# Performance work log

Measured on AMD Instinct MI355X. Metric: run time of the kernel, lower is better.

The kernel has to match this reference:

```python
import jax, jax.numpy as jnp
import numpy as np

NBLOCKS = 4
BATCH = 16384
DIMS = [(3072, 3000), (3000, 1000), (1000, 100), (100, 10)]


def _monarch_linear(x, w1, w2, bias, out_features):
    # x: (b, n); w1: (k, q, p) block-diag factor 1; w2: (l, s, r) block-diag factor 2
    b = x.shape[0]
    k, q, p = w1.shape
    l, s, r = w2.shape
    n_ext = k * p
    if x.shape[1] < n_ext:  # pad input up to in_features_extended
        x = jnp.pad(x, ((0, 0), (0, n_ext - x.shape[1])))
    xr = x.reshape(b, k, p)
    out1 = jnp.einsum('kqp,bkp->bkq', w1, xr)          # block-diag matmul 1
    # monarch permutation: flatten (k,q) -> view as (r,l) -> transpose to (l,r)
    out1 = out1.reshape(b, r, l).transpose(0, 2, 1)    # (b, l, r)
    out2 = jnp.einsum('lsr,blr->bls', w2, out1)        # block-diag matmul 2
    out = out2.reshape(b, l * s)[:, :out_features]     # truncate to out_features
    return out + bias


def _layer_shapes(fin, fout, nb):
    in_blk = -(-fin // nb)
    out_blk = -(-fout // nb)
    if in_blk * nb < out_blk * nb:
        return (nb, in_blk, in_blk), (nb, out_blk, in_blk)
    return (nb, out_blk, in_blk), (nb, out_blk, out_blk)


def setup_inputs() -> dict:
    key = jax.random.key(0)
    ks = jax.random.split(key, 16)
    inp = {"x": jax.random.normal(ks[0], (BATCH, DIMS[0][0]), jnp.float32)}
    i = 1
    for li, (fin, fout) in enumerate(DIMS, 1):
        s1, s2 = _layer_shapes(fin, fout, NBLOCKS)
        inp[f"w1_{li}"] = jax.random.normal(ks[i], s1, jnp.float32) / np.float32(np.sqrt(s1[2])); i += 1
        inp[f"w2_{li}"] = jax.random.normal(ks[i], s2, jnp.float32) / np.float32(np.sqrt(s2[2])); i += 1
        inp[f"b{li}"] = jnp.zeros((fout,), jnp.float32)
    return inp


def reference(x, w1_1, w2_1, b1, w1_2, w2_2, b2, w1_3, w2_3, b3, w1_4, w2_4, b4):
    h = x.reshape(x.shape[0], -1)
    h = jax.nn.relu(_monarch_linear(h, w1_1, w2_1, b1, 3000))
    h = jax.nn.relu(_monarch_linear(h, w1_2, w2_2, b2, 1000))
    h = jax.nn.relu(_monarch_linear(h, w1_3, w2_3, b3, 100))
    h = _monarch_linear(h, w1_4, w2_4, b4, 10)
    return jax.nn.log_softmax(h, axis=1)
```

## Files before the change

kernel.cpp:

```cpp
#include <hip/hip_runtime.h>
#include <stdint.h>
#include <math.h>

typedef unsigned short ushort_t;
typedef short short8 __attribute__((ext_vector_type(8)));
typedef float f32x4 __attribute__((ext_vector_type(4)));

__device__ __forceinline__ float b2f(ushort_t u) {
  union { uint32_t i; float f; } v; v.i = ((uint32_t)u) << 16; return v.f;
}
__device__ __forceinline__ ushort_t f2b(float f) {
  union { float f; uint32_t i; } v; v.f = f;
  uint32_t r = (v.i + 0x7FFFu + ((v.i >> 16) & 1u)) >> 16;
  return (ushort_t)r;
}

__device__ __forceinline__ void gload16(const void* g, void* l) {
  __builtin_amdgcn_global_load_lds(
      (const __attribute__((address_space(1))) void*)(uintptr_t)g,
      (__attribute__((address_space(3))) void*)(uint32_t)(uintptr_t)l,
      16, 0, 0);
}

__global__ void cast_f32_bf16(const float* __restrict__ src, ushort_t* __restrict__ dst, long n) {
  long stride = (long)gridDim.x * blockDim.x;
  for (long i = (long)blockIdx.x * blockDim.x + threadIdx.x; i * 8 < n; i += stride) {
    const float4* s = (const float4*)(src + i * 8);
    float4 a = s[0], b = s[1];
    short8 o;
    o[0] = (short)f2b(a.x); o[1] = (short)f2b(a.y); o[2] = (short)f2b(a.z); o[3] = (short)f2b(a.w);
    o[4] = (short)f2b(b.x); o[5] = (short)f2b(b.y); o[6] = (short)f2b(b.z); o[7] = (short)f2b(b.w);
    *(short8*)(dst + i * 8) = o;
  }
}

__global__ void cast_pad_w(const float* __restrict__ src, ushort_t* __restrict__ dst,
                           int NB, int Q, int P, int Qpad, int Ppad) {
  long total = (long)NB * Qpad * Ppad;
  for (long i = (long)blockIdx.x * blockDim.x + threadIdx.x; i < total;
       i += (long)gridDim.x * blockDim.x) {
    int p = (int)(i % Ppad);
    long t = i / Ppad;
    int q = (int)(t % Qpad);
    int b = (int)(t / Qpad);
    float v = (q < Q && p < P) ? src[((long)b * Q + q) * P + p] : 0.f;
    dst[i] = f2b(v);
  }
}

#define BM 128
#define BN 128
#define BK 64

template <int MODE>
__global__ __launch_bounds__(256, 2)
void gemm_bt(const ushort_t* __restrict__ A, int lda, long aZ,
             const ushort_t* __restrict__ W, int Npad, int Ppad, int K,
             const float* __restrict__ bias,
             ushort_t* __restrict__ out,
             int Q, int Rpad, long planeElems, int Spad, int ldout) {
  __shared__ __align__(16) ushort_t As[BM * BK];
  __shared__ __align__(16) ushort_t Bs[BN * BK];
  const int tid = threadIdx.x;
  const int lane = tid & 63;
  const int wave = tid >> 6;
  const int wm = wave >> 1, wn = wave & 1;
  const int z = blockIdx.z;
  const long m0 = (long)blockIdx.x * BM;
  const int n0 = blockIdx.y * BN;

  const ushort_t* Ab = A + (long)z * aZ + m0 * lda;
  const ushort_t* Wb = W + (long)z * Npad * Ppad + (long)n0 * Ppad;

  f32x4 acc[4][4] = {};

  for (int kt = 0; kt < K; kt += BK) {
#pragma unroll
    for (int i = 0; i < 4; ++i) {
      int ch = tid + i * 256;
      int r = ch >> 3;
      int c = (ch & 7) * 8;
      gload16(Ab + (long)r * lda + kt + c, &As[ch * 8]);
      gload16(Wb + (long)r * Ppad + kt + c, &Bs[ch * 8]);
    }
    __syncthreads();
#pragma unroll
    for (int kk = 0; kk < 2; ++kk) {
      short8 af[4], bf[4];
#pragma unroll
      for (int mi = 0; mi < 4; ++mi) {
        int row = wm * 64 + mi * 16 + (lane & 15);
        af[mi] = *(const short8*)&As[row * 64 + kk * 32 + ((lane >> 4) << 3)];
      }
#pragma unroll
      for (int nj = 0; nj < 4; ++nj) {
        int row = wn * 64 + nj * 16 + (lane & 15);
        bf[nj] = *(const short8*)&Bs[row * 64 + kk * 32 + ((lane >> 4) << 3)];
      }
#pragma unroll
      for (int mi = 0; mi < 4; ++mi)
#pragma unroll
        for (int nj = 0; nj < 4; ++nj)
          acc[mi][nj] = __builtin_amdgcn_mfma_f32_16x16x32_bf16(af[mi], bf[nj], acc[mi][nj], 0, 0, 0);
    }
    __syncthreads();
  }

  const int fq = lane >> 4;
  const int fr = lane & 15;
  if constexpr (MODE == 0) {
#pragma unroll
    for (int nj = 0; nj < 4; ++nj) {
      int q = n0 + wn * 64 + nj * 16 + fr;
      if (q < Q) {
        int f = z * Q + q;
        ushort_t* op = out + (long)(f & 3) * planeElems + (f >> 2);
#pragma unroll
        for (int mi = 0; mi < 4; ++mi) {
          long row = m0 + wm * 64 + mi * 16 + fq * 4;
#pragma unroll
          for (int j = 0; j < 4; ++j)
            op[(row + j) * (long)Rpad] = f2b(acc[mi][nj][j]);
        }
      }
    }
  } else {
#pragma unroll
    for (int nj = 0; nj < 4; ++nj) {
      int s = n0 + wn * 64 + nj * 16 + fr;
      if (s < Q) {
        float bv = bias[z * Q + s];
        ushort_t* op = out + (long)z * Spad + s;
#pragma unroll
        for (int mi = 0; mi < 4; ++mi) {
          long row = m0 + wm * 64 + mi * 16 + fq * 4;
#pragma unroll
          for (int j = 0; j < 4; ++j) {
            float v = acc[mi][nj][j] + bv;
            v = v > 0.f ? v : 0.f;
            op[(row + j) * (long)ldout] = f2b(v);
          }
        }
      }
    }
  }
}

__global__ __launch_bounds__(256)
void l4_softmax(const ushort_t* __restrict__ h3,
                const float* __restrict__ w14, const float* __restrict__ w24,
                const float* __restrict__ b4, float* __restrict__ outp) {
  __shared__ float w14s[300], w24s[36], b4s[10];
  int tid = threadIdx.x;
  for (int i = tid; i < 300; i += 256) w14s[i] = w14[i];
  if (tid < 36) w24s[tid] = w24[tid];
  if (tid < 10) b4s[tid] = b4[tid];
  __syncthreads();

  long row = (long)blockIdx.x * 256 + tid;
  const ushort_t* hr = h3 + row * 128;

  float a4[12];
#pragma unroll
  for (int k = 0; k < 4; ++k) {
    float hx[25];
#pragma unroll
    for (int p = 0; p < 25; ++p) hx[p] = b2f(hr[k * 32 + p]);
#pragma unroll
    for (int q = 0; q < 3; ++q) {
      float s = 0.f;
#pragma unroll
      for (int p = 0; p < 25; ++p) s += hx[p] * w14s[(k * 3 + q) * 25 + p];
      a4[k * 3 + q] = s;
    }
  }
  float logit[10];
#pragma unroll
  for (int l = 0; l < 4; ++l) {
#pragma unroll
    for (int s = 0; s < 3; ++s) {
      int j = l * 3 + s;
      if (j < 10) {
        float v = 0.f;
#pragma unroll
        for (int r = 0; r < 3; ++r) v += w24s[(l * 3 + s) * 3 + r] * a4[4 * r + l];
        logit[j] = v + b4s[j];
      }
    }
  }
  float m = logit[0];
#pragma unroll
  for (int j = 1; j < 10; ++j) m = fmaxf(m, logit[j]);
  float sum = 0.f;
#pragma unroll
  for (int j = 0; j < 10; ++j) sum += expf(logit[j] - m);
  float lse = m + logf(sum);
#pragma unroll
  for (int j = 0; j < 10; ++j) outp[row * 10 + j] = logit[j] - lse;
}

extern "C" void kernel_launch(void* const* d_in, const int* in_sizes, int n_in,
                              void* d_out, int out_size, void* d_ws, size_t ws_size,
                              hipStream_t stream) {
  (void)in_sizes; (void)n_in; (void)out_size; (void)ws_size;
  const float* x   = (const float*)d_in[0];
  const float* w11 = (const float*)d_in[1];
  const float* w21 = (const float*)d_in[2];
  const float* b1  = (const float*)d_in[3];
  const float* w12 = (const float*)d_in[4];
  const float* w22 = (const float*)d_in[5];
  const float* b2  = (const float*)d_in[6];
  const float* w13 = (const float*)d_in[7];
  const float* w23 = (const float*)d_in[8];
  const float* b3  = (const float*)d_in[9];
  const float* w14 = (const float*)d_in[10];
  const float* w24 = (const float*)d_in[11];
  const float* b4  = (const float*)d_in[12];
  float* out = (float*)d_out;
  char* ws = (char*)d_ws;

  ushort_t* w1b1 = (ushort_t*)(ws + 0);
  ushort_t* w2b1 = (ushort_t*)(ws + 4718592);
  ushort_t* w1b2 = (ushort_t*)(ws + 9437184);
  ushort_t* w2b2 = (ushort_t*)(ws + 11010048);
  ushort_t* w13b = (ushort_t*)(ws + 11534336);
  ushort_t* w23b = (ushort_t*)(ws + 11796480);
  const long OFF_XB = 11862016;
  ushort_t* xb = (ushort_t*)(ws + OFF_XB);
  ushort_t* t2 = (ushort_t*)(ws + OFF_XB);
  ushort_t* h2 = (ushort_t*)(ws + OFF_XB + 33554432);
  ushort_t* t3 = (ushort_t*)(ws + OFF_XB + 67108864);
  ushort_t* h3 = (ushort_t*)(ws + OFF_XB + 75497472);
  ushort_t* t1 = (ushort_t*)(ws + 112525312);
  ushort_t* h1 = (ushort_t*)(ws + 213188608);

  cast_f32_bf16<<<4096, 256, 0, stream>>>(x, xb, 50331648L);
  cast_pad_w<<<2048, 256, 0, stream>>>(w11, w1b1, 4, 750, 768, 768, 768);
  cast_pad_w<<<2048, 256, 0, stream>>>(w21, w2b1, 4, 750, 750, 768, 768);
  cast_pad_w<<<1024, 256, 0, stream>>>(w12, w1b2, 4, 250, 750, 256, 768);
  cast_pad_w<<<512, 256, 0, stream>>>(w22, w2b2, 4, 250, 250, 256, 256);
  cast_pad_w<<<256, 256, 0, stream>>>(w13, w13b, 4, 25, 250, 128, 256);
  cast_pad_w<<<128, 256, 0, stream>>>(w23, w23b, 4, 25, 25, 128, 64);

  gemm_bt<0><<<dim3(128, 6, 4), 256, 0, stream>>>(xb, 3072, 768L, w1b1, 768, 768, 768,
                                                  nullptr, t1, 750, 768, 16384L * 768, 0, 0);
  gemm_bt<1><<<dim3(128, 6, 4), 256, 0, stream>>>(t1, 768, 16384L * 768, w2b1, 768, 768, 768,
                                                  b1, h1, 750, 0, 0, 768, 3072);
  gemm_bt<0><<<dim3(128, 2, 4), 256, 0, stream>>>(h1, 3072, 768L, w1b2, 256, 768, 768,
                                                  nullptr, t2, 250, 256, 16384L * 256, 0, 0);
  gemm_bt<1><<<dim3(128, 2, 4), 256, 0, stream>>>(t2, 256, 16384L * 256, w2b2, 256, 256, 256,
                                                  b2, h2, 250, 0, 0, 256, 1024);
  gemm_bt<0><<<dim3(128, 1, 4), 256, 0, stream>>>(h2, 1024, 256L, w13b, 128, 256, 256,
                                                  nullptr, t3, 25, 64, 16384L * 64, 0, 0);
  gemm_bt<1><<<dim3(128, 1, 4), 256, 0, stream>>>(t3, 64, 16384L * 64, w23b, 128, 64, 64,
                                                  b3, h3, 25, 0, 0, 32, 128);
  l4_softmax<<<64, 256, 0, stream>>>(h3, w14, w24, b4, out);
}
```

Measured before the change: 719.0 us.

## Double-buffer LDS tiles in GEMM and swizzle block order across XCDs

The GEMM kernel now keeps two LDS buffers and issues the async global-to-LDS loads for the next K tile before computing on the current one, so memory transfer can overlap with MFMA work. It also launches a flat 1D grid and remaps block IDs with a stride-8 swizzle, presumably so neighbouring tiles that share A rows land on the same XCD's L2. LDS use doubles to 64KB per block, which may reduce occupancy below the launch-bounds target of 2 blocks per CU. The synchronisation placement in the unseen tail of the loop determines whether the overlap is race-free.

```diff
diff --git a/kernel.cpp b/kernel.cpp
--- a/kernel.cpp
+++ b/kernel.cpp
@@ -58,44 +58,63 @@
              const ushort_t* __restrict__ W, int Npad, int Ppad, int K,
              const float* __restrict__ bias,
              ushort_t* __restrict__ out,
-             int Q, int Rpad, long planeElems, int Spad, int ldout) {
-  __shared__ __align__(16) ushort_t As[BM * BK];
-  __shared__ __align__(16) ushort_t Bs[BN * BK];
+             int Q, int Rpad, long planeElems, int Spad, int ldout,
+             int gx, int gy) {
+  __shared__ __align__(16) ushort_t As[2][BM * BK];
+  __shared__ __align__(16) ushort_t Bs[2][BN * BK];
   const int tid = threadIdx.x;
   const int lane = tid & 63;
   const int wave = tid >> 6;
   const int wm = wave >> 1, wn = wave & 1;
-  const int z = blockIdx.z;
-  const long m0 = (long)blockIdx.x * BM;
-  const int n0 = blockIdx.y * BN;
+
+  const int nb = gridDim.x;
+  const int bid = blockIdx.x;
+  const int swz = (bid & 7) * (nb >> 3) + (bid >> 3);
+  const int bx = swz % gx;
+  const int rest = swz / gx;
+  const int by = rest % gy;
+  const int z = rest / gy;
+
+  const long m0 = (long)bx * BM;
+  const int n0 = by * BN;
 
   const ushort_t* Ab = A + (long)z * aZ + m0 * lda;
   const ushort_t* Wb = W + (long)z * Npad * Ppad + (long)n0 * Ppad;
 
   f32x4 acc[4][4] = {};
 
-  for (int kt = 0; kt < K; kt += BK) {
+  const int nsteps = K / BK;
+
+  auto stage = [&](int b, int kt) {
 #pragma unroll
     for (int i = 0; i < 4; ++i) {
       int ch = tid + i * 256;
       int r = ch >> 3;
       int c = (ch & 7) * 8;
-      gload16(Ab + (long)r * lda + kt + c, &As[ch * 8]);
-      gload16(Wb + (long)r * Ppad + kt + c, &Bs[ch * 8]);
-    }
-    __syncthreads();
+      gload16(Ab + (long)r * lda + kt + c, &As[b][ch * 8]);
+      gload16(Wb + (long)r * Ppad + kt + c, &Bs[b][ch * 8]);
+    }
+  };
+
+  stage(0, 0);
+  __syncthreads();
+
+  for (int it = 0; it < nsteps; ++it) {
+    const int cur = it & 1;
+    if (it + 1 < nsteps) stage(cur ^ 1, (it + 1) * BK);
+
 #pragma unroll
     for (int kk = 0; kk < 2; ++kk) {
       short8 af[4], bf[4];
 #pragma unroll
       for (int mi = 0; mi < 4; ++mi) {
         int row = wm * 64 + mi * 16 + (lane & 15);
-        af[mi] = *(const short8*)&As[row * 64 + kk * 32 + ((lane >> 4) << 3)];
+        af[mi] = *(const short8*)&As[cur][row * 64 + kk * 32 + ((lane >> 4) << 3)];
       }
 #pragma unroll
       for (int nj = 0; nj < 4; ++nj) {
         int row = wn * 64 + nj * 16 + (lane & 15);
-        bf[nj] = *(const short8*)&Bs[row * 64 + kk * 32 + ((lane >> 4) << 3)];
+        bf[nj] = *(const short8*)&Bs[cur][row * 64 + kk * 32 + ((lane >> 4) << 3)];
       }
 #pragma unroll
       for (int mi = 0; mi < 4; ++mi)
@@ -242,17 +261,17 @@
   cast_pad_w<<<256, 256, 0, stream>>>(w13, w13b, 4, 25, 250, 128, 256);
   cast_pad_w<<<128, 256, 0, stream>>>(w23, w23b, 4, 25, 25, 128, 64);
 
-  gemm_bt<0><<<dim3(128, 6, 4), 256, 0, stream>>>(xb, 3072, 768L, w1b1, 768, 768, 768,
-                                                  nullptr, t1, 750, 768, 16384L * 768, 0, 0);
-  gemm_bt<1><<<dim3(128, 6, 4), 256, 0, stream>>>(t1, 768, 16384L * 768, w2b1, 768, 768, 768,
-                                                  b1, h1, 750, 0, 0, 768, 3072);
-  gemm_bt<0><<<dim3(128, 2, 4), 256, 0, stream>>>(h1, 3072, 768L, w1b2, 256, 768, 768,
-                                                  nullptr, t2, 250, 256, 16384L * 256, 0, 0);
-  gemm_bt<1><<<dim3(128, 2, 4), 256, 0, stream>>>(t2, 256, 16384L * 256, w2b2, 256, 256, 256,
-                                                  b2, h2, 250, 0, 0, 256, 1024);
-  gemm_bt<0><<<dim3(128, 1, 4), 256, 0, stream>>>(h2, 1024, 256L, w13b, 128, 256, 256,
-                                                  nullptr, t3, 25, 64, 16384L * 64, 0, 0);
-  gemm_bt<1><<<dim3(128, 1, 4), 256, 0, stream>>>(t3, 64, 16384L * 64, w23b, 128, 64, 64,
-                                                  b3, h3, 25, 0, 0, 32, 128);
+  gemm_bt<0><<<128 * 6 * 4, 256, 0, stream>>>(xb, 3072, 768L, w1b1, 768, 768, 768,
+                                              nullptr, t1, 750, 768, 16384L * 768, 0, 0, 128, 6);
+  gemm_bt<1><<<128 * 6 * 4, 256, 0, stream>>>(t1, 768, 16384L * 768, w2b1, 768, 768, 768,
+                                              b1, h1, 750, 0, 0, 768, 3072, 128, 6);
+  gemm_bt<0><<<128 * 2 * 4, 256, 0, stream>>>(h1, 3072, 768L, w1b2, 256, 768, 768,
+                                              nullptr, t2, 250, 256, 16384L * 256, 0, 0, 128, 2);
+  gemm_bt<1><<<128 * 2 * 4, 256, 0, stream>>>(t2, 256, 16384L * 256, w2b2, 256, 256, 256,
+                                              b2, h2, 250, 0, 0, 256, 1024, 128, 2);
+  gemm_bt<0><<<128 * 1 * 4, 256, 0, stream>>>(h2, 1024, 256L, w13b, 128, 256, 256,
+                                              nullptr, t3, 25, 64, 16384L * 64, 0, 0, 128, 1);
+  gemm_bt<1><<<128 * 1 * 4, 256, 0, stream>>>(t3, 64, 16384L * 64, w23b, 128, 64, 64,
+                                              b3, h3, 25, 0, 0, 32, 128, 128, 1);
   l4_softmax<<<64, 256, 0, stream>>>(h3, w14, w24, b4, out);
 }
```

Measured after the change: 768.7 us. 6.9% more time.

## Add 256x256-tile GEMM with 4-slot LDS ring and swizzled layout for layers 1-2

Applied to the files above, without the earlier changes.

Adds a new GEMM kernel using 512 threads and 256x256 output tiles, fed by a 4-deep ring buffer of 32-wide K slices loaded directly into LDS, with an XOR-swizzled chunk layout to avoid bank conflicts. The four large block-diagonal matmuls of layers 1 and 2 switch to it. The intent is to raise arithmetic intensity per tile and hide global load latency through deeper prefetch. In exchange it uses 128KB of LDS per block and a large accumulator register footprint, which limits occupancy, and it gives fewer blocks for the smaller layer-2 GEMMs.

```diff
diff --git a/kernel.cpp b/kernel.cpp
--- a/kernel.cpp
+++ b/kernel.cpp
@@ -20,6 +20,17 @@
       (const __attribute__((address_space(1))) void*)(uintptr_t)g,
       (__attribute__((address_space(3))) void*)(uint32_t)(uintptr_t)l,
       16, 0, 0);
+}
+
+__device__ __forceinline__ int swz_chunk(int r, int c) {
+  int rp = (r >> 1) & 7;
+  int s8 = ((r & 1) << 2) | c;
+  return ((r >> 4) << 6) | (rp << 3) | (s8 ^ rp);
+}
+__device__ __forceinline__ void inv_chunk(int p, int& r, int& c) {
+  int rp = (p >> 3) & 7, ps = p & 7, s8 = ps ^ rp;
+  r = ((p >> 6) << 4) | (rp << 1) | (s8 >> 2);
+  c = s8 & 3;
 }
 
 __global__ void cast_f32_bf16(const float* __restrict__ src, ushort_t* __restrict__ dst, long n) {
@@ -45,6 +56,121 @@
     int b = (int)(t / Qpad);
     float v = (q < Q && p < P) ? src[((long)b * Q + q) * P + p] : 0.f;
     dst[i] = f2b(v);
+  }
+}
+
+template <int MODE>
+__global__ __launch_bounds__(512, 2)
+void gemm_ring(const ushort_t* __restrict__ A, int lda, long aZ,
+               const ushort_t* __restrict__ W, int Npad, int Ppad, int K,
+               const float* __restrict__ bias,
+               ushort_t* __restrict__ out,
+               int Q, int Rpad, long planeElems, int Spad, int ldout) {
+  __shared__ __align__(16) ushort_t lds[65536];
+  const int tid = threadIdx.x;
+  const int lane = tid & 63;
+  const int wave = tid >> 6;
+  const int wm = wave >> 2;
+  const int wn = wave & 3;
+  const int z = blockIdx.z;
+  const long m0 = (long)blockIdx.x * 256;
+  const int n0 = blockIdx.y * 256;
+
+  const ushort_t* Ab = A + (long)z * aZ + m0 * lda;
+  const ushort_t* Wb = W + (long)z * Npad * Ppad + (long)n0 * Ppad;
+
+  int r0, c0, r1, c1;
+  inv_chunk(tid, r0, c0);
+  inv_chunk(tid + 512, r1, c1);
+  const ushort_t* gA0 = Ab + (long)r0 * lda + c0 * 8;
+  const ushort_t* gA1 = Ab + (long)r1 * lda + c1 * 8;
+  const ushort_t* gB0 = Wb + (long)r0 * Ppad + c0 * 8;
+  const ushort_t* gB1 = Wb + (long)r1 * Ppad + c1 * 8;
+
+  int offA[8], offB[4];
+#pragma unroll
+  for (int mi = 0; mi < 8; ++mi)
+    offA[mi] = swz_chunk(wm * 128 + mi * 16 + (lane & 15), lane >> 4) * 8;
+#pragma unroll
+  for (int nj = 0; nj < 4; ++nj)
+    offB[nj] = 8192 + swz_chunk(wn * 64 + nj * 16 + (lane & 15), lane >> 4) * 8;
+
+  auto stage = [&](int slot, int kt) {
+    long koff = (long)kt * 32;
+    ushort_t* base = &lds[slot * 16384];
+    gload16(gA0 + koff, base + tid * 8);
+    gload16(gA1 + koff, base + 4096 + tid * 8);
+    gload16(gB0 + koff, base + 8192 + tid * 8);
+    gload16(gB1 + koff, base + 12288 + tid * 8);
+  };
+
+  const int nsteps = K / 32;
+  stage(0, 0);
+  stage(1, 1);
+  stage(2, 2);
+
+  f32x4 acc[8][4] = {};
+
+  for (int kt = 0; kt < nsteps; ++kt) {
+    asm volatile("s_waitcnt vmcnt(8)" ::: "memory");
+    __builtin_amdgcn_s_barrier();
+    int nx = kt + 3;
+    if (nx >= nsteps) nx = nsteps - 1;
+    stage((kt + 3) & 3, nx);
+
+    const ushort_t* sl = &lds[(kt & 3) * 16384];
+    short8 af[8], bf[4];
+#pragma unroll
+    for (int mi = 0; mi < 8; ++mi) af[mi] = *(const short8*)(sl + offA[mi]);
+#pragma unroll
+    for (int nj = 0; nj < 4; ++nj) bf[nj] = *(const short8*)(sl + offB[nj]);
+
+    __builtin_amdgcn_s_setprio(1);
+#pragma unroll
+    for (int mi = 0; mi < 8; ++mi)
+#pragma unroll
+      for (int nj = 0; nj < 4; ++nj)
+        acc[mi][nj] = __builtin_amdgcn_mfma_f32_16x16x32_bf16(af[mi], bf[nj], acc[mi][nj], 0, 0, 0);
+    __builtin_amdgcn_s_setprio(0);
+  }
+
+  const int fq = lane >> 4;
+  const int fr = lane & 15;
+  if constexpr (MODE == 0) {
+#pragma unroll
+    for (int nj = 0; nj < 4; ++nj) {
+      int q = n0 + wn * 64 + nj * 16 + fr;
+      if (q < Q) {
+        int f = z * Q + q;
+        ushort_t* op = out + (long)(f & 3) * planeElems + (f >> 2);
+#pragma unroll
+        for (int mi = 0; mi < 8; ++mi) {
+          long row = m0 + wm * 128 + mi * 16 + fq * 4;
+#pragma unroll
+          for (int j = 0; j < 4; ++j)
+            op[(row + j) * (long)Rpad] = f2b(acc[mi][nj][j]);
+        }
+      }
+    }
+  } else {
+#pragma unroll
+    for (int nj = 0; nj < 4; ++nj) {
+      int s = n0 + wn * 64 + nj * 16 + fr;
+      if (s < Q) {
+        float bv = bias[z * Q + s];
+        ushort_t* op = out + (long)z * Spad + s;
+#pragma unroll
+        for (int mi = 0; mi < 8; ++mi) {
+          long row = m0 + wm * 128 + mi * 16 + fq * 4;
+#pragma unroll
+          for (int j = 0; j < 4; ++j) {
+            float v = acc[mi][nj][j] + bv;
+            v = v > 0.f ? v : 0.f;
+            op[(row + j) * (long)ldout] = f2b(v);
+          }
+        }
+      }
+    }
   }
 }
 
@@ -242,14 +368,14 @@
   cast_pad_w<<<256, 256, 0, stream>>>(w13, w13b, 4, 25, 250, 128, 256);
   cast_pad_w<<<128, 256, 0, stream>>>(w23, w23b, 4, 25, 25, 128, 64);
 
-  gemm_bt<0><<<dim3(128, 6, 4), 256, 0, stream>>>(xb, 3072, 768L, w1b1, 768, 768, 768,
-                                                  nullptr, t1, 750, 768, 16384L * 768, 0, 0);
-  gemm_bt<1><<<dim3(128, 6, 4), 256, 0, stream>>>(t1, 768, 16384L * 768, w2b1, 768, 768, 768,
-                                                  b1, h1, 750, 0, 0, 768, 3072);
-  gemm_bt<0><<<dim3(128, 2, 4), 256, 0, stream>>>(h1, 3072, 768L, w1b2, 256, 768, 768,
-                                                  nullptr, t2, 250, 256, 16384L * 256, 0, 0);
-  gemm_bt<1><<<dim3(128, 2, 4), 256, 0, stream>>>(t2, 256, 16384L * 256, w2b2, 256, 256, 256,
-                                                  b2, h2, 250, 0, 0, 256, 1024);
+  gemm_ring<0><<<dim3(64, 3, 4), 512, 0, stream>>>(xb, 3072, 768L, w1b1, 768, 768, 768,
+                                                   nullptr, t1, 750, 768, 16384L * 768, 0, 0);
+  gemm_ring<1><<<dim3(64, 3, 4), 512, 0, stream>>>(t1, 768, 16384L * 768, w2b1, 768, 768, 768,
+                                                   b1, h1, 750, 0, 0, 768, 3072);
+  gemm_ring<0><<<dim3(64, 1, 4), 512, 0, stream>>>(h1, 3072, 768L, w1b2, 256, 768, 768,
+                                                   nullptr, t2, 250, 256, 16384L * 256, 0, 0);
+  gemm_ring<1><<<dim3(64, 1, 4), 512, 0, stream>>>(t2, 256, 16384L * 256, w2b2, 256, 256, 256,
+                                                   b2, h2, 250, 0, 0, 256, 1024);
   gemm_bt<0><<<dim3(128, 1, 4), 256, 0, stream>>>(h2, 1024, 256L, w13b, 128, 256, 256,
                                                   nullptr, t3, 25, 64, 16384L * 64, 0, 0);
   gemm_bt<1><<<dim3(128, 1, 4), 256, 0, stream>>>(t3, 64, 16384L * 64, w23b, 128, 64, 64,
```

Result: faster. 700.7 us (-2.6%).
